# Optimization experiments

Hardware: AMD Instinct MI355X
Metric: run time of the kernel (lower is better)

Reference implementation:

```python
import jax, jax.numpy as jnp
import numpy as np

N, P, IN, HID, HEADS, OUT, E = 8192, 3, 256, 64, 8, 64, 262144
HD = HEADS * HID


def _gat(h, fc, al, ar, bias, src, dst):
    # DGL GATConv forward (no dropout), returns (elu(out) [N,H,D], attention [E,H])
    feat = (h @ fc).reshape(N, HEADS, HID)          # [N,H,D]
    el = (feat * al).sum(-1)                        # [N,H]
    er = (feat * ar).sum(-1)                        # [N,H]
    e = jax.nn.leaky_relu(el[src] + er[dst], negative_slope=0.2)  # [E,H]
    emax = jax.ops.segment_max(e, dst, num_segments=N)            # [N,H]
    ee = jnp.exp(e - emax[dst])
    denom = jax.ops.segment_sum(ee, dst, num_segments=N)          # [N,H]
    a = ee / denom[dst]                                           # edge softmax over dst
    rst = jax.ops.segment_sum(a[:, :, None] * feat[src], dst, num_segments=N)  # [N,H,D]
    out = jax.nn.elu(rst + bias)
    return out, a


def setup_inputs():
    key = jax.random.key(0)
    ks = jax.random.split(key, 12)
    s = 0.05
    return {
        "h": jax.random.normal(ks[0], (N, IN), jnp.float32),
        "edge_src": jax.random.randint(ks[1], (P, E), 0, N, jnp.int32),
        "edge_dst": jax.random.randint(ks[2], (P, E), 0, N, jnp.int32),
        "gat_fc": jax.random.normal(ks[3], (P, IN, HD), jnp.float32) * s,
        "attn_l": jax.random.normal(ks[4], (P, HEADS, HID), jnp.float32) * s,
        "attn_r": jax.random.normal(ks[5], (P, HEADS, HID), jnp.float32) * s,
        "gat_bias": jnp.zeros((P, HEADS, HID), jnp.float32),
        "sa_w1": jax.random.normal(ks[6], (HD, 128), jnp.float32) * s,
        "sa_b1": jnp.zeros((128,), jnp.float32),
        "sa_w2": jax.random.normal(ks[7], (128, 1), jnp.float32) * s,
        "pred_w": jax.random.normal(ks[8], (HD, OUT), jnp.float32) * s,
        "pred_b": jnp.zeros((OUT,), jnp.float32),
    }


def reference(h, edge_src, edge_dst, gat_fc, attn_l, attn_r, gat_bias,
              sa_w1, sa_b1, sa_w2, pred_w, pred_b):
    zp_list, alpha_list = [], []
    for p in range(P):
        z_p, a_p = _gat(h, gat_fc[p], attn_l[p], attn_r[p], gat_bias[p],
                        edge_src[p], edge_dst[p])
        zp_list.append(z_p.reshape(N, HD))          # flatten(start_dim=1)
        alpha_list.append(a_p.mean(axis=1))         # [E], mean over heads
    zp = jnp.stack(zp_list, axis=1)                 # [N,P,HD]

    # Semantic attention
    w = (zp @ sa_w1 + sa_b1) @ sa_w2                # [N,P,1]
    w = jax.nn.leaky_relu(w, negative_slope=0.01).mean(axis=0)  # [P,1]
    beta = jax.nn.softmax(w, axis=0)                # [P,1]

    # Dense adjacency accumulation of edge attention weights
    atten = jnp.zeros((N, N), jnp.float32)
    for p in range(P):
        vals = alpha_list[p] * beta[p, 0]
        atten = atten.at[edge_src[p], edge_dst[p]].add(vals)

    z = (beta[None, :, :] * zp).sum(axis=1)         # [N,HD]
    out = z @ pred_w + pred_b                       # [N,OUT]
    return out, atten
```

## Files before the change

### kernel.cpp

```cpp
#include <hip/hip_runtime.h>
#include <math.h>

#define NN    8192
#define PP    3
#define INF_  256
#define HID_  64
#define HEADS 8
#define OUTF  64
#define NE    262144
#define HD    512
#define DEGCAP 128
#define NB    4
#define DOFF  (4 * NN)
#define SOFF  (12 * NN)
#define POFF  (4 * NN + 1)

typedef __attribute__((ext_vector_type(8))) short short8;
typedef __attribute__((ext_vector_type(4))) float f32x4;

__device__ __forceinline__ unsigned short f2bf(float f) {
    unsigned u = __float_as_uint(f);
    unsigned r = u + 0x7fffu + ((u >> 16) & 1u);
    return (unsigned short)(r >> 16);
}
__device__ __forceinline__ float bf2f_lo(unsigned v) { return __uint_as_float(v << 16); }
__device__ __forceinline__ float bf2f_hi(unsigned v) { return __uint_as_float(v & 0xffff0000u); }

__device__ __forceinline__ void beta_reg(const float* __restrict__ wsum,
                                         float& rb0, float& rb1, float& rb2) {
    int lane = threadIdx.x & 63;
    float s0 = wsum[lane], s1 = wsum[64 + lane], s2 = wsum[128 + lane];
#pragma unroll
    for (int off = 32; off > 0; off >>= 1) {
        s0 += __shfl_down(s0, off);
        s1 += __shfl_down(s1, off);
        s2 += __shfl_down(s2, off);
    }
    float t0 = __shfl(s0, 0), t1 = __shfl(s1, 0), t2 = __shfl(s2, 0);
    float w0 = t0 / (float)NN, w1 = t1 / (float)NN, w2 = t2 / (float)NN;
    float m  = fmaxf(w0, fmaxf(w1, w2));
    float e0 = expf(w0 - m), e1 = expf(w1 - m), e2 = expf(w2 - m);
    float ss = e0 + e1 + e2;
    rb0 = e0 / ss; rb1 = e1 / ss; rb2 = e2 / ss;
}

__global__ __launch_bounds__(256) void cast_count(
        const float* __restrict__ h, const float* __restrict__ fc,
        const int* __restrict__ esrc, const int* __restrict__ edst,
        unsigned short* __restrict__ hb, unsigned short* __restrict__ fcT,
        int* __restrict__ counts ) {
    int b = blockIdx.x, t = threadIdx.x;
    if (b < 2048) {
        int i = b * 256 + t;
        float4 v = *(const float4*)(h + (size_t)i * 4);
        ushort4 o = { f2bf(v.x), f2bf(v.y), f2bf(v.z), f2bf(v.w) };
        *(ushort4*)(hb + (size_t)i * 4) = o;
    } else if (b < 2048 + 1536) {
        int i = (b - 2048) * 256 + t;
        if (i < PP * INF_ * HD) {
            int p = i / (INF_ * HD);
            int rem = i - p * INF_ * HD;
            int k = rem / HD;
            int n = rem - k * HD;
            fcT[(size_t)p * HD * INF_ + (size_t)n * INF_ + k] = f2bf(fc[i]);
        }
    } else {
        int i = (b - 3584) * 256 + t;
        int4 s4 = ((const int4*)esrc)[i];
        int4 d4 = ((const int4*)edst)[i];
        int p = i >> 16;
        int base = p * DOFF;
        atomicAdd(&counts[base + (d4.x << 2) + (s4.x >> 11)], 1);
        atomicAdd(&counts[base + (d4.y << 2) + (s4.y >> 11)], 1);
        atomicAdd(&counts[base + (d4.z << 2) + (s4.z >> 11)], 1);
        atomicAdd(&counts[base + (d4.w << 2) + (s4.w >> 11)], 1);
        atomicAdd(&counts[SOFF + s4.x], 1);
        atomicAdd(&counts[SOFF + s4.y], 1);
        atomicAdd(&counts[SOFF + s4.z], 1);
        atomicAdd(&counts[SOFF + s4.w], 1);
    }
}

__global__ __launch_bounds__(1024) void scan_vw(
        const int* __restrict__ counts, int* __restrict__ offsets,
        int* __restrict__ cursor, const float* __restrict__ w1,
        const float* __restrict__ b1, const float* __restrict__ w2,
        float* __restrict__ v ) {
    int t = threadIdx.x;
    if (blockIdx.x == 4) {
        if (t < HD) {
            float s = 0.f;
            for (int k = 0; k < 128; ++k) s += w1[t * 128 + k] * w2[k];
            v[t] = s;
        } else if (t == HD) {
            float c = 0.f;
            for (int k = 0; k < 128; ++k) c += b1[k] * w2[k];
            v[HD] = c;
        }
        return;
    }
    __shared__ int sh[1024];
    if (blockIdx.x == 3) {
        const int* cnt = counts + SOFF;
        int* offs = offsets + 3 * POFF;
        int* cur  = cursor + SOFF;
        int loc[8];
        int s = 0;
#pragma unroll
        for (int i = 0; i < 8; ++i) { loc[i] = cnt[t * 8 + i]; s += loc[i]; }
        sh[t] = s;
        __syncthreads();
        for (int off = 1; off < 1024; off <<= 1) {
            int vv = (t >= off) ? sh[t - off] : 0;
            __syncthreads();
            sh[t] += vv;
            __syncthreads();
        }
        int run = sh[t] - s;
#pragma unroll
        for (int i = 0; i < 8; ++i) {
            offs[t * 8 + i] = run;
            cur[t * 8 + i]  = run;
            run += loc[i];
        }
        if (t == 1023) offs[NN] = run;
        return;
    }
    int seg = blockIdx.x;
    const int* cnt = counts + seg * DOFF;
    int* offs = offsets + seg * POFF;
    int* cur  = cursor + seg * DOFF;
    int loc[32];
    int s = 0;
#pragma unroll
    for (int i = 0; i < 32; ++i) { loc[i] = cnt[t * 32 + i]; s += loc[i]; }
    sh[t] = s;
    __syncthreads();
    for (int off = 1; off < 1024; off <<= 1) {
        int vv = (t >= off) ? sh[t - off] : 0;
        __syncthreads();
        sh[t] += vv;
        __syncthreads();
    }
    int run = sh[t] - s;
#pragma unroll
    for (int i = 0; i < 32; ++i) {
        offs[t * 32 + i] = run;
        cur[t * 32 + i]  = run;
        run += loc[i];
    }
    if (t == 1023) offs[DOFF] = run;
}

#define LDK 72
__global__ __launch_bounds__(256) void scatter_gemm(
        const int* __restrict__ esrc, const int* __restrict__ edst,
        int* __restrict__ cursor, int* __restrict__ ssrc_sorted,
        int2* __restrict__ spair,
        const unsigned short* __restrict__ hb,
        const unsigned short* __restrict__ fcT,
        const float* __restrict__ al_all,
        const float* __restrict__ ar_all,
        unsigned short* __restrict__ featb,
        float* __restrict__ el,
        float* __restrict__ er) {
    __shared__ unsigned short As[64 * LDK];
    __shared__ unsigned short Bs[64 * LDK];
    int tid = threadIdx.x;
    if (blockIdx.x < 3072) {
        int i = blockIdx.x * 256 + tid;
        int p = i >> 18;
        int s = esrc[i], d = edst[i];
        int pos = atomicAdd(&cursor[p * DOFF + (d << 2) + (s >> 11)], 1);
        ssrc_sorted[(size_t)p * NE + pos] = s;
        int pos2 = atomicAdd(&cursor[SOFF + s], 1);
        int2 pr; pr.x = p * NE + pos; pr.y = d;
        spair[pos2] = pr;
        return;
    }
    int g  = blockIdx.x - 3072;
    int p  = g >> 10;
    int n0 = (g & 7) * 64;
    int m0 = ((g >> 3) & 127) * 64;
    const unsigned short* Bt = fcT + (size_t)p * HD * INF_;
    unsigned short* C = featb + (size_t)p * NN * HD;
    int wv   = tid >> 6, lane = tid & 63;
    int row  = tid >> 2, kc = (tid & 3) * 8;
    int l16  = lane & 15, quad = lane >> 4;
    int mw   = wv * 16;
    f32x4 acc[4] = {{0.f,0.f,0.f,0.f},{0.f,0.f,0.f,0.f},
                    {0.f,0.f,0.f,0.f},{0.f,0.f,0.f,0.f}};
    for (int k0 = 0; k0 < INF_; k0 += 64) {
        const unsigned short* ha = &hb[(size_t)(m0 + row) * INF_ + k0 + kc];
        const unsigned short* ba = &Bt[(size_t)(n0 + row) * INF_ + k0 + kc];
        *(short8*)&As[row * LDK + kc]      = *(const short8*)ha;
        *(short8*)&As[row * LDK + kc + 32] = *(const short8*)(ha + 32);
        *(short8*)&Bs[row * LDK + kc]      = *(const short8*)ba;
        *(short8*)&Bs[row * LDK + kc + 32] = *(const short8*)(ba + 32);
        __syncthreads();
        short8 af0 = *(short8*)&As[(mw + l16) * LDK + quad * 8];
        short8 af1 = *(short8*)&As[(mw + l16) * LDK + 32 + quad * 8];
#pragma unroll
        for (int nt = 0; nt < 4; ++nt) {
            short8 bf0 = *(short8*)&Bs[(nt * 16 + l16) * LDK + quad * 8];
            acc[nt] = __builtin_amdgcn_mfma_f32_16x16x32_bf16(af0, bf0, acc[nt], 0, 0, 0);
            short8 bf1 = *(short8*)&Bs[(nt * 16 + l16) * LDK + 32 + quad * 8];
            acc[nt] = __builtin_amdgcn_mfma_f32_16x16x32_bf16(af1, bf1, acc[nt], 0, 0, 0);
        }
        __syncthreads();
    }
#pragma unroll
    for (int nt = 0; nt < 4; ++nt) {
#pragma unroll
        for (int r = 0; r < 4; ++r) {
            C[(size_t)(m0 + mw + quad * 4 + r) * HD + n0 + nt * 16 + l16] =
                f2bf(acc[nt][r]);
        }
    }
    int hidx = n0 >> 6;
    float alv[4], arv[4];
#pragma unroll
    for (int nt = 0; nt < 4; ++nt) {
        alv[nt] = al_all[p * HD + n0 + nt * 16 + l16];
        arv[nt] = ar_all[p * HD + n0 + nt * 16 + l16];
    }
    float* elp = el + (size_t)p * NN * HEADS;
    float* erp = er + (size_t)p * NN * HEADS;
#pragma unroll
    for (int r = 0; r < 4; ++r) {
        float pe = acc[0][r] * alv[0] + acc[1][r] * alv[1] +
                   acc[2][r] * alv[2] + acc[3][r] * alv[3];
        float pr = acc[0][r] * arv[0] + acc[1][r] * arv[1] +
                   acc[2][r] * arv[2] + acc[3][r] * arv[3];
#pragma unroll
        for (int m = 1; m < 16; m <<= 1) {
            pe += __shfl_xor(pe, m);
            pr += __shfl_xor(pr, m);
        }
        if (l16 == 0) {
            int node = m0 + mw + quad * 4 + r;
            elp[node * HEADS + hidx] = pe;
            erp[node * HEADS + hidx] = pr;
        }
    }
}

__global__ __launch_bounds__(256) void fused_attn_rst(
        const int* __restrict__ ssrc_sorted, const int* __restrict__ offsets_all,
        const float* __restrict__ el, const float* __restrict__ er,
        const unsigned short* __restrict__ featb,
        const float* __restrict__ bias_all, const float* __restrict__ v,
        float* __restrict__ alpha_all ,
        unsigned short* __restrict__ zpb,
        float* __restrict__ wsum ) {
    __shared__ float sh_e[4][DEGCAP * 8];
    __shared__ int   sh_src[4][DEGCAP];
    int wv = threadIdx.x >> 6, lane = threadIdx.x & 63;
    int gid = blockIdx.x * 4 + wv;
    int n = gid & (NN - 1);
    int p = gid >> 13;
    const int* srcrow  = ssrc_sorted + (size_t)p * NE;
    const int* offs    = offsets_all + p * POFF;
    const float* elp   = el + (size_t)p * NN * HEADS;
    const float* erp   = er + (size_t)p * NN * HEADS;
    const unsigned short* feat = featb + (size_t)p * NN * HD;
    int start = offs[n * 4];
    int deg = offs[n * 4 + 4] - start;
    if (deg > DEGCAP) deg = DEGCAP;

    float4 r0 = *(const float4*)(erp + n * 8);
    float4 r1 = *(const float4*)(erp + n * 8 + 4);
    for (int t = lane; t < deg; t += 64) {
        int s = srcrow[start + t];
        sh_src[wv][t] = s;
        float4 l0 = *(const float4*)(elp + s * 8);
        float4 l1 = *(const float4*)(elp + s * 8 + 4);
        float sc[8] = {l0.x + r0.x, l0.y + r0.y, l0.z + r0.z, l0.w + r0.w,
                       l1.x + r1.x, l1.y + r1.y, l1.z + r1.z, l1.w + r1.w};
#pragma unroll
        for (int hh = 0; hh < 8; ++hh) {
            float x = sc[hh];
            sh_e[wv][t * 8 + hh] = x > 0.f ? x : 0.2f * x;
        }
    }
    __syncthreads();

    int h = lane >> 3;
    {
        int j = lane & 7;
        float m = -INFINITY;
        for (int t = j; t < deg; t += 8) m = fmaxf(m, sh_e[wv][t * 8 + h]);
#pragma unroll
        for (int off = 4; off; off >>= 1) m = fmaxf(m, __shfl_xor(m, off));
        float ssum = 0.f;
        for (int t = j; t < deg; t += 8) {
            float ee = __expf(sh_e[wv][t * 8 + h] - m);
            sh_e[wv][t * 8 + h] = ee;
            ssum += ee;
        }
#pragma unroll
        for (int off = 4; off; off >>= 1) ssum += __shfl_xor(ssum, off);
        float inv = 1.f / ssum;
        for (int t = j; t < deg; t += 8) sh_e[wv][t * 8 + h] *= inv;
    }
    __syncthreads();

    for (int t = lane; t < deg; t += 64) {
        float s = 0.f;
#pragma unroll
        for (int hh = 0; hh < 8; ++hh) s += sh_e[wv][t * 8 + hh];
        alpha_all[(size_t)p * NE + start + t] = s * 0.125f;
    }

    int c = lane * 8;
    float acc[8] = {0.f, 0.f, 0.f, 0.f, 0.f, 0.f, 0.f, 0.f};
#define FMA8(F, KI) { \
        float a_ = sh_e[wv][(KI) * 8 + h]; \
        acc[0] += a_ * bf2f_lo((F).x); acc[1] += a_ * bf2f_hi((F).x); \
        acc[2] += a_ * bf2f_lo((F).y); acc[3] += a_ * bf2f_hi((F).y); \
        acc[4] += a_ * bf2f_lo((F).z); acc[5] += a_ * bf2f_hi((F).z); \
        acc[6] += a_ * bf2f_lo((F).w); acc[7] += a_ * bf2f_hi((F).w); }
    int k = 0;
    for (; k + 4 <= deg; k += 4) {
        int s0 = sh_src[wv][k],     s1 = sh_src[wv][k + 1];
        int s2 = sh_src[wv][k + 2], s3 = sh_src[wv][k + 3];
        uint4 f0 = *(const uint4*)&feat[(size_t)s0 * HD + c];
        uint4 f1 = *(const uint4*)&feat[(size_t)s1 * HD + c];
        uint4 f2 = *(const uint4*)&feat[(size_t)s2 * HD + c];
        uint4 f3 = *(const uint4*)&feat[(size_t)s3 * HD + c];
        FMA8(f0, k); FMA8(f1, k + 1); FMA8(f2, k + 2); FMA8(f3, k + 3);
    }
    for (; k < deg; ++k) {
        int s = sh_src[wv][k];
        uint4 f = *(const uint4*)&feat[(size_t)s * HD + c];
        FMA8(f, k);
    }
#undef FMA8
    const float* bias = bias_all + p * HD;
    float4 b0 = *(const float4*)(bias + c);
    float4 b1 = *(const float4*)(bias + c + 4);
    float z[8];
    z[0] = acc[0] + b0.x; z[1] = acc[1] + b0.y; z[2] = acc[2] + b0.z; z[3] = acc[3] + b0.w;
    z[4] = acc[4] + b1.x; z[5] = acc[5] + b1.y; z[6] = acc[6] + b1.z; z[7] = acc[7] + b1.w;
#pragma unroll
    for (int i = 0; i < 8; ++i) z[i] = z[i] > 0.f ? z[i] : expm1f(z[i]);
    uint4 zo;
    zo.x = (unsigned)f2bf(z[0]) | ((unsigned)f2bf(z[1]) << 16);
    zo.y = (unsigned)f2bf(z[2]) | ((unsigned)f2bf(z[3]) << 16);
    zo.z = (unsigned)f2bf(z[4]) | ((unsigned)f2bf(z[5]) << 16);
    zo.w = (unsigned)f2bf(z[6]) | ((unsigned)f2bf(z[7]) << 16);
    *(uint4*)&zpb[(size_t)n * (PP * HD) + p * HD + c] = zo;

    float4 v0 = *(const float4*)(v + c);
    float4 v1 = *(const float4*)(v + c + 4);
    float part = z[0] * v0.x + z[1] * v0.y + z[2] * v0.z + z[3] * v0.w +
                 z[4] * v1.x + z[5] * v1.y + z[6] * v1.z + z[7] * v1.w;
#pragma unroll
    for (int off = 32; off > 0; off >>= 1) part += __shfl_down(part, off);
    if (lane == 0) {
        float w = part + v[HD];
        w = w > 0.f ? w : 0.01f * w;
        atomicAdd(&wsum[p * 64 + (n & 63)], w);
    }
}

#define K5R 16
__global__ __launch_bounds__(256) void final_atten(
        const unsigned short* __restrict__ zpb, const float* __restrict__ wsum,
        const float* __restrict__ pw, const float* __restrict__ pb,
        const int2* __restrict__ spair, const int* __restrict__ soffs,
        const float* __restrict__ alpha,
        float* __restrict__ out, float* __restrict__ atten) {
    __shared__ float buf[NN];
    float b0, b1, b2;
    beta_reg(wsum, b0, b1, b2);
    int tid = threadIdx.x;
    if (blockIdx.x < NN) {
        int srow = blockIdx.x;
        f32x4 zero = {0.f, 0.f, 0.f, 0.f};
        for (int j = tid; j < NN / 4; j += 256) ((f32x4*)buf)[j] = zero;
        __syncthreads();
        int s0 = soffs[srow], s1 = soffs[srow + 1];
        for (int k = s0 + tid; k < s1; k += 256) {
            int2 pr = spair[k];
            int pp = pr.x >> 18;
            float bsel = pp == 0 ? b0 : (pp == 1 ? b1 : b2);
            atomicAdd(&buf[pr.y], alpha[pr.x] * bsel);
        }
        __syncthreads();
        float* orow = atten + (size_t)srow * NN;
        for (int j = tid * 4; j < NN; j += 1024) {
            f32x4 v = *(f32x4*)(buf + j);
            __builtin_nontemporal_store(v, (f32x4*)(orow + j));
        }
    } else {
        int n0 = (blockIdx.x - NN) * K5R;
        float* zt = buf;
        int c = tid * 2;
#pragma unroll
        for (int r = 0; r < K5R; ++r) {
            const unsigned short* zr = zpb + (size_t)(n0 + r) * (PP * HD);
            unsigned u0 = *(const unsigned*)(zr + c);
            unsigned u1 = *(const unsigned*)(zr + HD + c);
            unsigned u2 = *(const unsigned*)(zr + 2 * HD + c);
            zt[r * HD + c]     = b0 * bf2f_lo(u0) + b1 * bf2f_lo(u1) + b2 * bf2f_lo(u2);
            zt[r * HD + c + 1] = b0 * bf2f_hi(u0) + b1 * bf2f_hi(u1) + b2 * bf2f_hi(u2);
        }
        __syncthreads();
        int o = tid & 63, rg = tid >> 6;
        float a0 = 0.f, a1 = 0.f, a2 = 0.f, a3 = 0.f;
        for (int j = 0; j < HD; ++j) {
            float pwj = pw[j * 64 + o];
            a0 += zt[(rg * 4 + 0) * HD + j] * pwj;
            a1 += zt[(rg * 4 + 1) * HD + j] * pwj;
            a2 += zt[(rg * 4 + 2) * HD + j] * pwj;
            a3 += zt[(rg * 4 + 3) * HD + j] * pwj;
        }
        float bo = pb[o];
        out[(size_t)(n0 + rg * 4 + 0) * 64 + o] = a0 + bo;
        out[(size_t)(n0 + rg * 4 + 1) * 64 + o] = a1 + bo;
        out[(size_t)(n0 + rg * 4 + 2) * 64 + o] = a2 + bo;
        out[(size_t)(n0 + rg * 4 + 3) * 64 + o] = a3 + bo;
    }
}

extern "C" void kernel_launch(void* const* d_in, const int* in_sizes, int n_in,
                              void* d_out, int out_size, void* d_ws, size_t ws_size,
                              hipStream_t stream) {
    const float* h    = (const float*)d_in[0];
    const int*   esrc = (const int*)d_in[1];
    const int*   edst = (const int*)d_in[2];
    const float* fc   = (const float*)d_in[3];
    const float* al   = (const float*)d_in[4];
    const float* ar   = (const float*)d_in[5];
    const float* bias = (const float*)d_in[6];
    const float* w1   = (const float*)d_in[7];
    const float* b1   = (const float*)d_in[8];
    const float* w2   = (const float*)d_in[9];
    const float* pw   = (const float*)d_in[10];
    const float* pb   = (const float*)d_in[11];
    float* out   = (float*)d_out;
    float* atten = out + (size_t)NN * OUTF;

    char* ws = (char*)d_ws;
    size_t off = 0;
    auto alloc = [&](size_t bytes) {
        void* p = ws + off;
        off = (off + bytes + 255) & ~(size_t)255;
        return p;
    };
    unsigned short* zpb   = (unsigned short*)alloc(sizeof(short) * (size_t)NN * PP * HD);
    unsigned short* featb = (unsigned short*)alloc(sizeof(short) * (size_t)PP * NN * HD);
    unsigned short* hb  = (unsigned short*)alloc(sizeof(short) * (size_t)NN * INF_);
    unsigned short* fcT = (unsigned short*)alloc(sizeof(short) * (size_t)PP * HD * INF_);
    float*  el      = (float*)alloc(sizeof(float) * PP * NN * HEADS);
    float*  er      = (float*)alloc(sizeof(float) * PP * NN * HEADS);
    float*  alpha   = (float*)alloc(sizeof(float) * (size_t)PP * NE);
    int*    counts  = (int*)alloc(sizeof(int) * 13 * NN);
    float*  wsum    = (float*)alloc(sizeof(float) * 3 * 64);
    int*    offsets = (int*)alloc(sizeof(int) * (3 * POFF + NN + 1));
    int*    cursor  = (int*)alloc(sizeof(int) * 13 * NN);
    int*    ssrc_sorted = (int*)alloc(sizeof(int) * (size_t)PP * NE);
    int2*   spair   = (int2*)alloc(sizeof(int2) * (size_t)PP * NE);
    float*  vbuf    = (float*)alloc(sizeof(float) * (HD + 1));

    (void)hipMemsetAsync(counts, 0, sizeof(int) * 13 * NN + 1024, stream);

    cast_count<<<2048 + 1536 + 768, 256, 0, stream>>>(
        h, fc, esrc, edst, hb, fcT, counts);

    scan_vw<<<5, 1024, 0, stream>>>(counts, offsets, cursor, w1, b1, w2, vbuf);

    scatter_gemm<<<6144, 256, 0, stream>>>(
        esrc, edst, cursor, ssrc_sorted, spair,
        hb, fcT, al, ar, featb, el, er);

    fused_attn_rst<<<NN * PP / 4, 256, 0, stream>>>(
        ssrc_sorted, offsets, el, er, featb, bias, vbuf, alpha, zpb, wsum);

    final_atten<<<NN + NN / K5R, 256, 0, stream>>>(
        zpb, wsum, pw, pb, spair, offsets + 3 * POFF, alpha, out, atten);
}
```

Before: 642.4 us.

## Split attention kernel into score and aggregation passes; use finer source buckets

The fused edge-softmax plus aggregation kernel is split into two kernels. The first computes the softmax scores and writes them per edge and head to a new global buffer, and the second reloads them and aggregates the gathered features. Each kernel should have lower register and LDS pressure and higher occupancy, at the cost of an extra round trip of about 25 MB of scores through memory and one more launch. Separately, source-range buckets per destination grow from 4 to 8, which should give finer source locality within each destination's edge list, but makes the count and scan arrays larger and removes register caching in the scan.

```diff
diff --git a/kernel.cpp b/kernel.cpp
--- a/kernel.cpp
+++ b/kernel.cpp
@@ -10,10 +10,10 @@
 #define NE    262144
 #define HD    512
 #define DEGCAP 128
-#define NB    4
-#define DOFF  (4 * NN)
-#define SOFF  (12 * NN)
-#define POFF  (4 * NN + 1)
+#define NB    8
+#define DOFF  (NB * NN)
+#define SOFF  (3 * DOFF)
+#define POFF  (NB * NN + 1)
 
 typedef __attribute__((ext_vector_type(8))) short short8;
 typedef __attribute__((ext_vector_type(4))) float f32x4;
@@ -70,10 +70,10 @@
         int4 d4 = ((const int4*)edst)[i];
         int p = i >> 16;
         int base = p * DOFF;
-        atomicAdd(&counts[base + (d4.x << 2) + (s4.x >> 11)], 1);
-        atomicAdd(&counts[base + (d4.y << 2) + (s4.y >> 11)], 1);
-        atomicAdd(&counts[base + (d4.z << 2) + (s4.z >> 11)], 1);
-        atomicAdd(&counts[base + (d4.w << 2) + (s4.w >> 11)], 1);
+        atomicAdd(&counts[base + (d4.x << 3) + (s4.x >> 10)], 1);
+        atomicAdd(&counts[base + (d4.y << 3) + (s4.y >> 10)], 1);
+        atomicAdd(&counts[base + (d4.z << 3) + (s4.z >> 10)], 1);
+        atomicAdd(&counts[base + (d4.w << 3) + (s4.w >> 10)], 1);
         atomicAdd(&counts[SOFF + s4.x], 1);
         atomicAdd(&counts[SOFF + s4.y], 1);
         atomicAdd(&counts[SOFF + s4.z], 1);
@@ -130,10 +130,8 @@
     const int* cnt = counts + seg * DOFF;
     int* offs = offsets + seg * POFF;
     int* cur  = cursor + seg * DOFF;
-    int loc[32];
     int s = 0;
-#pragma unroll
-    for (int i = 0; i < 32; ++i) { loc[i] = cnt[t * 32 + i]; s += loc[i]; }
+    for (int i = 0; i < 64; ++i) s += cnt[t * 64 + i];
     sh[t] = s;
     __syncthreads();
     for (int off = 1; off < 1024; off <<= 1) {
@@ -143,11 +141,11 @@
         __syncthreads();
     }
     int run = sh[t] - s;
-#pragma unroll
-    for (int i = 0; i < 32; ++i) {
-        offs[t * 32 + i] = run;
-        cur[t * 32 + i]  = run;
-        run += loc[i];
+    for (int i = 0; i < 64; ++i) {
+        int c = cnt[t * 64 + i];
+        offs[t * 64 + i] = run;
+        cur[t * 64 + i]  = run;
+        run += c;
     }
     if (t == 1023) offs[DOFF] = run;
 }
@@ -171,7 +169,7 @@
         int i = blockIdx.x * 256 + tid;
         int p = i >> 18;
         int s = esrc[i], d = edst[i];
-        int pos = atomicAdd(&cursor[p * DOFF + (d << 2) + (s >> 11)], 1);
+        int pos = atomicAdd(&cursor[p * DOFF + (d << 3) + (s >> 10)], 1);
         ssrc_sorted[(size_t)p * NE + pos] = s;
         int pos2 = atomicAdd(&cursor[SOFF + s], 1);
         int2 pr; pr.x = p * NE + pos; pr.y = d;
@@ -245,12 +243,75 @@
     }
 }
 
-__global__ __launch_bounds__(256) void fused_attn_rst(
+__global__ __launch_bounds__(256) void attn_scores(
         const int* __restrict__ ssrc_sorted, const int* __restrict__ offsets_all,
         const float* __restrict__ el, const float* __restrict__ er,
+        float* __restrict__ alpha_all, float* __restrict__ escore ) {
+    __shared__ float sh_e[4][DEGCAP * 8];
+    int wv = threadIdx.x >> 6, lane = threadIdx.x & 63;
+    int gid = blockIdx.x * 4 + wv;
+    int n = gid & (NN - 1);
+    int p = gid >> 13;
+    const int* srcrow  = ssrc_sorted + (size_t)p * NE;
+    const int* offs    = offsets_all + p * POFF;
+    const float* elp   = el + (size_t)p * NN * HEADS;
+    const float* erp   = er + (size_t)p * NN * HEADS;
+    int start = offs[n * NB];
+    int deg = offs[n * NB + NB] - start;
+    if (deg > DEGCAP) deg = DEGCAP;
+
+    float4 r0 = *(const float4*)(erp + n * 8);
+    float4 r1 = *(const float4*)(erp + n * 8 + 4);
+    for (int t = lane; t < deg; t += 64) {
+        int s = srcrow[start + t];
+        float4 l0 = *(const float4*)(elp + s * 8);
+        float4 l1 = *(const float4*)(elp + s * 8 + 4);
+        float sc[8] = {l0.x + r0.x, l0.y + r0.y, l0.z + r0.z, l0.w + r0.w,
+                       l1.x + r1.x, l1.y + r1.y, l1.z + r1.z, l1.w + r1.w};
+#pragma unroll
+        for (int hh = 0; hh < 8; ++hh) {
+            float x = sc[hh];
+            sh_e[wv][t * 8 + hh] = x > 0.f ? x : 0.2f * x;
+        }
+    }
+    __syncthreads();
+
+    int h = lane >> 3;
+    {
+        int j = lane & 7;
+        float m = -INFINITY;
+        for (int t = j; t < deg; t += 8) m = fmaxf(m, sh_e[wv][t * 8 + h]);
+#pragma unroll
+        for (int off = 4; off; off >>= 1) m = fmaxf(m, __shfl_xor(m, off));
+        float ssum = 0.f;
+        for (int t = j; t < deg; t += 8) {
+            float ee = __expf(sh_e[wv][t * 8 + h] - m);
+            sh_e[wv][t * 8 + h] = ee;
+            ssum += ee;
+        }
+#pragma unroll
+        for (int off = 4; off; off >>= 1) ssum += __shfl_xor(ssum, off);
+        float inv = 1.f / ssum;
+        for (int t = j; t < deg; t += 8) sh_e[wv][t * 8 + h] *= inv;
+    }
+    __syncthreads();
+
+    for (int t = lane; t < deg; t += 64) {
+        float4 e0 = *(const float4*)&sh_e[wv][t * 8];
+        float4 e1 = *(const float4*)&sh_e[wv][t * 8 + 4];
+        float s = e0.x + e0.y + e0.z + e0.w + e1.x + e1.y + e1.z + e1.w;
+        alpha_all[(size_t)p * NE + start + t] = s * 0.125f;
+        float* eo = escore + (size_t)(p * NE + start + t) * 8;
+        *(float4*)eo = e0;
+        *(float4*)(eo + 4) = e1;
+    }
+}
+
+__global__ __launch_bounds__(256) void attn_aggr(
+        const int* __restrict__ ssrc_sorted, const int* __restrict__ offsets_all,
+        const float* __restrict__ escore,
         const unsigned short* __restrict__ featb,
         const float* __restrict__ bias_all, const float* __restrict__ v,
-        float* __restrict__ alpha_all ,
         unsigned short* __restrict__ zpb,
         float* __restrict__ wsum ) {
     __shared__ float sh_e[4][DEGCAP * 8];
@@ -261,57 +322,20 @@
     int p = gid >> 13;
     const int* srcrow  = ssrc_sorted + (size_t)p * NE;
     const int* offs    = offsets_all + p * POFF;
-    const float* elp   = el + (size_t)p * NN * HEADS;
-    const float* erp   = er + (size_t)p * NN * HEADS;
     const unsigned short* feat = featb + (size_t)p * NN * HD;
-    int start = offs[n * 4];
-    int deg = offs[n * 4 + 4] - start;
+    int start = offs[n * NB];
+    int deg = offs[n * NB + NB] - start;
     if (deg > DEGCAP) deg = DEGCAP;
 
-    float4 r0 = *(const float4*)(erp + n * 8);
-    float4 r1 = *(const float4*)(erp + n * 8 + 4);
     for (int t = lane; t < deg; t += 64) {
-        int s = srcrow[start + t];
-        sh_src[wv][t] = s;
-        float4 l0 = *(const float4*)(elp + s * 8);
-        float4 l1 = *(const float4*)(elp + s * 8 + 4);
-        float sc[8] = {l0.x + r0.x, l0.y + r0.y, l0.z + r0.z, l0.w + r0.w,
-                       l1.x + r1.x, l1.y + r1.y, l1.z + r1.z, l1.w + r1.w};
-#pragma unroll
-        for (int hh = 0; hh < 8; ++hh) {
-            float x = sc[hh];
-            sh_e[wv][t * 8 + hh] = x > 0.f ? x : 0.2f * x;
-        }
+        sh_src[wv][t] = srcrow[start + t];
+        const float* ei = escore + (size_t)(p * NE + start + t) * 8;
+        *(float4*)&sh_e[wv][t * 8]     = *(const float4*)ei;
+        *(float4*)&sh_e[wv][t * 8 + 4] = *(const float4*)(ei + 4);
     }
     __syncthreads();
 
     int h = lane >> 3;
-    {
-        int j = lane & 7;
-        float m = -INFINITY;
-        for (int t = j; t < deg; t += 8) m = fmaxf(m, sh_e[wv][t * 8 + h]);
-#pragma unroll
-        for (int off = 4; off; off >>= 1) m = fmaxf(m, __shfl_xor(m, off));
-        float ssum = 0.f;
-        for (int t = j; t < deg; t += 8) {
-            float ee = __expf(sh_e[wv][t * 8 + h] - m);
-            sh_e[wv][t * 8 + h] = ee;
-            ssum += ee;
-        }
-#pragma unroll
-        for (int off = 4; off; off >>= 1) ssum += __shfl_xor(ssum, off);
-        float inv = 1.f / ssum;
-        for (int t = j; t < deg; t += 8) sh_e[wv][t * 8 + h] *= inv;
-    }
-    __syncthreads();
-
-    for (int t = lane; t < deg; t += 64) {
-        float s = 0.f;
-#pragma unroll
-        for (int hh = 0; hh < 8; ++hh) s += sh_e[wv][t * 8 + hh];
-        alpha_all[(size_t)p * NE + start + t] = s * 0.125f;
-    }
-
     int c = lane * 8;
     float acc[8] = {0.f, 0.f, 0.f, 0.f, 0.f, 0.f, 0.f, 0.f};
 #define FMA8(F, KI) { \
@@ -456,15 +480,16 @@
     float*  el      = (float*)alloc(sizeof(float) * PP * NN * HEADS);
     float*  er      = (float*)alloc(sizeof(float) * PP * NN * HEADS);
     float*  alpha   = (float*)alloc(sizeof(float) * (size_t)PP * NE);
-    int*    counts  = (int*)alloc(sizeof(int) * 13 * NN);
+    float*  escore  = (float*)alloc(sizeof(float) * (size_t)PP * NE * 8);
+    int*    counts  = (int*)alloc(sizeof(int) * (3 * DOFF + NN));
     float*  wsum    = (float*)alloc(sizeof(float) * 3 * 64);
     int*    offsets = (int*)alloc(sizeof(int) * (3 * POFF + NN + 1));
-    int*    cursor  = (int*)alloc(sizeof(int) * 13 * NN);
+    int*    cursor  = (int*)alloc(sizeof(int) * (3 * DOFF + NN));
     int*    ssrc_sorted = (int*)alloc(sizeof(int) * (size_t)PP * NE);
     int2*   spair   = (int2*)alloc(sizeof(int2) * (size_t)PP * NE);
     float*  vbuf    = (float*)alloc(sizeof(float) * (HD + 1));
 
-    (void)hipMemsetAsync(counts, 0, sizeof(int) * 13 * NN + 1024, stream);
+    (void)hipMemsetAsync(counts, 0, sizeof(int) * (3 * DOFF + NN) + 1024, stream);
 
     cast_count<<<2048 + 1536 + 768, 256, 0, stream>>>(
         h, fc, esrc, edst, hb, fcT, counts);
@@ -475,8 +500,11 @@
         esrc, edst, cursor, ssrc_sorted, spair,
         hb, fcT, al, ar, featb, el, er);
 
-    fused_attn_rst<<<NN * PP / 4, 256, 0, stream>>>(
-        ssrc_sorted, offsets, el, er, featb, bias, vbuf, alpha, zpb, wsum);
+    attn_scores<<<NN * PP / 4, 256, 0, stream>>>(
+        ssrc_sorted, offsets, el, er, alpha, escore);
+
+    attn_aggr<<<NN * PP / 4, 256, 0, stream>>>(
+        ssrc_sorted, offsets, escore, featb, bias, vbuf, zpb, wsum);
 
     final_atten<<<NN + NN / K5R, 256, 0, stream>>>(
         zpb, wsum, pw, pb, spair, offsets + 3 * POFF, alpha, out, atten);
```

Measured after the change: 678.6 us. +5.6%, slower.
